# Kernel optimization log

Measured on AMD Instinct MI355X. Metric: run time of the kernel, lower is better.

## Reference

```python
import jax, jax.numpy as jnp
import numpy as np

FH, FW, CIN, COUT = 5, 5, 3, 16
PATCH = FH * FW * CIN  # 75
ALPHA = 1.0


def smooth_max(xk, axis):
    # alpha-softmax smooth maximum: sum(x * exp(alpha*x)) / sum(exp(alpha*x))
    w = jax.nn.softmax(ALPHA * xk, axis=axis)
    return jnp.sum(w * xk, axis=axis)


def setup_inputs() -> dict:
    key = jax.random.key(0)
    k_x, k_k1, k_k2 = jax.random.split(key, 3)
    B, Hout, Wout = 2, 220, 220
    x = jax.random.normal(k_x, (B, PATCH, Hout, Wout), dtype=jnp.float32)
    # xavier_uniform for kernel shape (fh, fw, cin, cout): fan_in=fh*fw*cin? torch treats
    # dims [..0]=fan stuff; a small uniform init is faithful enough for a numeric baseline.
    lim = float(np.sqrt(6.0 / (PATCH + COUT)))
    k1 = jax.random.uniform(k_k1, (FH, FW, CIN, COUT), jnp.float32, -lim, lim)
    k2 = jax.random.uniform(k_k2, (FH, FW, CIN, COUT), jnp.float32, -lim, lim)
    bias = jnp.zeros((COUT,), dtype=jnp.float32)
    return {"x": x, "k1": k1, "k2": k2, "bias": bias}


def reference(x, k1, k2, bias):
    # x: (B, patch_dim, Hout, Wout) unfolded patches
    k1f = k1.reshape(PATCH, COUT)  # (patch_dim, out_ch)
    k2f = k2.reshape(PATCH, COUT)
    # broadcast add: (B, patch_dim, out_ch, H, W)
    xk1 = x[:, :, None, :, :] + k1f[None, :, :, None, None]
    y11 = smooth_max(xk1, axis=1)  # (B, out_ch, H, W)
    xk2 = (-x)[:, :, None, :, :] + k2f[None, :, :, None, None]
    y22 = smooth_max(xk2, axis=1)
    return y11 + y22 + bias[None, :, None, None]
```

## Files before the change

### kernel.cpp

```cpp
#include <hip/hip_runtime.h>

#define HWD    48400
#define PATCHD 75
#define NPOS   96800

typedef __attribute__((ext_vector_type(8))) _Float16 f16x8;
typedef __attribute__((ext_vector_type(2))) __fp16   h16x2;
typedef __attribute__((ext_vector_type(4))) float    f32x4;

union U2 { h16x2 h; unsigned u; };
union UF { unsigned u[4]; f16x8 v; };

__global__ void smorph_build_tables(const float* __restrict__ k1,
                                    const float* __restrict__ k2,
                                    _Float16* __restrict__ tbl)
{
    int i = (int)blockIdx.x * 256 + (int)threadIdx.x;
    if (i >= 4 * 3 * 4 * 16 * 8) return;
    const int j = i & 7;
    const int c = (i >> 3) & 15;
    const int g = (i >> 7) & 3;
    const int t = i >> 9;
    const int s = t % 3;
    const int r = t / 3;
    const int k = 32 * s + 8 * g + j;
    float val = 0.f;
    if (k < PATCHD) {
        const float* kw = (r < 2) ? k1 : k2;
        const float w = kw[k * 16 + c];
        const float e = __expf(w);
        val = (r & 1) ? (w * e) : e;
    }
    tbl[i] = (_Float16)val;
}

__global__ __launch_bounds__(256, 4)
void smorph_mfma6(const float* __restrict__ x,
                  const _Float16* __restrict__ tbl,
                  const float* __restrict__ bias,
                  float* __restrict__ out)
{
    const int tid = (int)threadIdx.x;
    const int l   = tid & 63;
    const int w   = tid >> 6;
    const int g   = l >> 4;
    const int c   = l & 15;
    const int p0  = (int)blockIdx.x * 64 + w * 16;
    if (p0 >= NPOS) return;
    const int b   = (p0 >= HWD) ? 1 : 0;
    const int hw0 = p0 - b * HWD;

    const float* xb = x + (size_t)b * PATCHD * HWD + hw0 + c;
    const f16x8* tf = (const f16x8*)tbl;
    const int fbase = g * 16 + c;

    float xv[3][8];
    #pragma unroll
    for (int s = 0; s < 3; ++s)
        #pragma unroll
        for (int j = 0; j < 8; ++j) {
            int k = 32 * s + 8 * g + j;
            k = (k > PATCHD - 1) ? (PATCHD - 1) : k;
            xv[s][j] = xb[(size_t)k * HWD];
        }

    f32x4 aN1 = {0.f,0.f,0.f,0.f}, aD1 = {0.f,0.f,0.f,0.f};
    f32x4 aN2 = {0.f,0.f,0.f,0.f}, aD2 = {0.f,0.f,0.f,0.f};

    #pragma unroll
    for (int s = 0; s < 3; ++s) {
        const f16x8 a1f = tf[(0 * 3 + s) * 64 + fbase];
        const f16x8 b1f = tf[(1 * 3 + s) * 64 + fbase];
        const f16x8 a2f = tf[(2 * 3 + s) * 64 + fbase];
        const f16x8 b2f = tf[(3 * 3 + s) * 64 + fbase];

        float E[8], R[8];
        #pragma unroll
        for (int j = 0; j < 8; ++j) {
            E[j] = __expf(xv[s][j]);
            R[j] = __expf(-xv[s][j]);
        }

        UF fEx, fE, fRx, fR;
        #pragma unroll
        for (int jp = 0; jp < 4; ++jp) {
            const float x0 = xv[s][2*jp], x1 = xv[s][2*jp+1];
            U2 q;
            q.h = __builtin_amdgcn_cvt_pkrtz(E[2*jp] * x0,  E[2*jp+1] * x1);  fEx.u[jp] = q.u;
            q.h = __builtin_amdgcn_cvt_pkrtz(E[2*jp],       E[2*jp+1]);       fE.u[jp]  = q.u;
            q.h = __builtin_amdgcn_cvt_pkrtz(-R[2*jp] * x0, -R[2*jp+1] * x1); fRx.u[jp] = q.u;
            q.h = __builtin_amdgcn_cvt_pkrtz(R[2*jp],       R[2*jp+1]);       fR.u[jp]  = q.u;
        }

        aN1 = __builtin_amdgcn_mfma_f32_16x16x32_f16(a1f, fEx.v, aN1, 0, 0, 0);
        aN1 = __builtin_amdgcn_mfma_f32_16x16x32_f16(b1f, fE.v,  aN1, 0, 0, 0);
        aD1 = __builtin_amdgcn_mfma_f32_16x16x32_f16(a1f, fE.v,  aD1, 0, 0, 0);
        aN2 = __builtin_amdgcn_mfma_f32_16x16x32_f16(a2f, fRx.v, aN2, 0, 0, 0);
        aN2 = __builtin_amdgcn_mfma_f32_16x16x32_f16(b2f, fR.v,  aN2, 0, 0, 0);
        aD2 = __builtin_amdgcn_mfma_f32_16x16x32_f16(a2f, fR.v,  aD2, 0, 0, 0);
    }

    const float4 bsv = *(const float4*)(bias + 4 * g);
    float* ob = out + ((size_t)(b * 16 + 4 * g)) * HWD + hw0 + c;
    ob[0 * (size_t)HWD] = aN1[0] * __builtin_amdgcn_rcpf(aD1[0]) + aN2[0] * __builtin_amdgcn_rcpf(aD2[0]) + bsv.x;
    ob[1 * (size_t)HWD] = aN1[1] * __builtin_amdgcn_rcpf(aD1[1]) + aN2[1] * __builtin_amdgcn_rcpf(aD2[1]) + bsv.y;
    ob[2 * (size_t)HWD] = aN1[2] * __builtin_amdgcn_rcpf(aD1[2]) + aN2[2] * __builtin_amdgcn_rcpf(aD2[2]) + bsv.z;
    ob[3 * (size_t)HWD] = aN1[3] * __builtin_amdgcn_rcpf(aD1[3]) + aN2[3] * __builtin_amdgcn_rcpf(aD2[3]) + bsv.w;
}

extern "C" void kernel_launch(void* const* d_in, const int* in_sizes, int n_in,
                              void* d_out, int out_size, void* d_ws, size_t ws_size,
                              hipStream_t stream)
{
    const float* x    = (const float*)d_in[0];
    const float* k1   = (const float*)d_in[1];
    const float* k2   = (const float*)d_in[2];
    const float* bias = (const float*)d_in[3];
    float* out = (float*)d_out;
    _Float16* tbl = (_Float16*)d_ws;

    smorph_build_tables<<<(4 * 3 * 4 * 16 * 8 + 255) / 256, 256, 0, stream>>>(k1, k2, tbl);
    smorph_mfma6<<<(NPOS + 63) / 64, 256, 0, stream>>>(x, tbl, bias, out);
}
```

Measured before the change: 18.18 us.

## Convert to persistent grid-stride kernel with double-buffered x prefetch

Replaces the one-tile-per-block launch with a fixed grid of 512 persistent blocks that loop over tiles with a stride. Each block keeps the coefficient table fragments in registers and prefetches the next tile's x values into a second register buffer while it computes the current tile. The aim is to overlap global-load latency with exp and MFMA work and to stop reloading the table per tile. In exchange it uses more registers (occupancy hint lowered to 2) and gives load balancing over only about three tiles per block.

```diff
diff --git a/kernel.cpp b/kernel.cpp
--- a/kernel.cpp
+++ b/kernel.cpp
@@ -3,6 +3,8 @@
 #define HWD    48400
 #define PATCHD 75
 #define NPOS   96800
+#define NTILE  1513
+#define GRID   512
 
 typedef __attribute__((ext_vector_type(8))) _Float16 f16x8;
 typedef __attribute__((ext_vector_type(2))) __fp16   h16x2;
@@ -34,8 +36,8 @@
     tbl[i] = (_Float16)val;
 }
 
-__global__ __launch_bounds__(256, 4)
-void smorph_mfma6(const float* __restrict__ x,
+__global__ __launch_bounds__(256, 2)
+void smorph_mfma7(const float* __restrict__ x,
                   const _Float16* __restrict__ tbl,
                   const float* __restrict__ bias,
                   float* __restrict__ out)
@@ -45,67 +47,100 @@
     const int w   = tid >> 6;
     const int g   = l >> 4;
     const int c   = l & 15;
-    const int p0  = (int)blockIdx.x * 64 + w * 16;
-    if (p0 >= NPOS) return;
-    const int b   = (p0 >= HWD) ? 1 : 0;
-    const int hw0 = p0 - b * HWD;
 
-    const float* xb = x + (size_t)b * PATCHD * HWD + hw0 + c;
     const f16x8* tf = (const f16x8*)tbl;
     const int fbase = g * 16 + c;
+    f16x8 Tf[12];
+    #pragma unroll
+    for (int t = 0; t < 12; ++t) Tf[t] = tf[t * 64 + fbase];
 
-    float xv[3][8];
-    #pragma unroll
-    for (int s = 0; s < 3; ++s)
-        #pragma unroll
-        for (int j = 0; j < 8; ++j) {
-            int k = 32 * s + 8 * g + j;
-            k = (k > PATCHD - 1) ? (PATCHD - 1) : k;
-            xv[s][j] = xb[(size_t)k * HWD];
+    const float4 bsv = *(const float4*)(bias + 4 * g);
+
+    #define LOADX(dst, tt)                                                    \
+        {                                                                     \
+            int p0b_ = (tt) * 64;                                             \
+            if (p0b_ > NPOS - 64) p0b_ = NPOS - 64;                           \
+            const int p0_ = p0b_ + w * 16;                                    \
+            const int bb_ = (p0_ >= HWD) ? 1 : 0;                             \
+            const float* xb_ = x + (size_t)bb_ * PATCHD * HWD                 \
+                               + (p0_ - bb_ * HWD) + c;                       \
+            _Pragma("unroll")                                                 \
+            for (int s_ = 0; s_ < 3; ++s_)                                    \
+                _Pragma("unroll")                                             \
+                for (int j_ = 0; j_ < 8; ++j_) {                              \
+                    int k_ = 32 * s_ + 8 * g + j_;                            \
+                    k_ = (k_ > PATCHD - 1) ? (PATCHD - 1) : k_;               \
+                    (dst)[s_ * 8 + j_] = xb_[(size_t)k_ * HWD];               \
+                }                                                             \
         }
 
-    f32x4 aN1 = {0.f,0.f,0.f,0.f}, aD1 = {0.f,0.f,0.f,0.f};
-    f32x4 aN2 = {0.f,0.f,0.f,0.f}, aD2 = {0.f,0.f,0.f,0.f};
-
-    #pragma unroll
-    for (int s = 0; s < 3; ++s) {
-        const f16x8 a1f = tf[(0 * 3 + s) * 64 + fbase];
-        const f16x8 b1f = tf[(1 * 3 + s) * 64 + fbase];
-        const f16x8 a2f = tf[(2 * 3 + s) * 64 + fbase];
-        const f16x8 b2f = tf[(3 * 3 + s) * 64 + fbase];
-
-        float E[8], R[8];
-        #pragma unroll
-        for (int j = 0; j < 8; ++j) {
-            E[j] = __expf(xv[s][j]);
-            R[j] = __expf(-xv[s][j]);
+    #define COMPSTORE(src, tt)                                                \
+        {                                                                     \
+            f32x4 aN1 = {0.f,0.f,0.f,0.f}, aD1 = {0.f,0.f,0.f,0.f};          \
+            f32x4 aN2 = {0.f,0.f,0.f,0.f}, aD2 = {0.f,0.f,0.f,0.f};          \
+            _Pragma("unroll")                                                 \
+            for (int s_ = 0; s_ < 3; ++s_) {                                  \
+                float E[8], R[8];                                             \
+                _Pragma("unroll")                                             \
+                for (int j_ = 0; j_ < 8; ++j_) {                              \
+                    E[j_] = __expf((src)[s_ * 8 + j_]);                       \
+                    R[j_] = __expf(-(src)[s_ * 8 + j_]);                      \
+                }                                                             \
+                UF fEx, fE, fRx, fR;                                          \
+                _Pragma("unroll")                                             \
+                for (int jp = 0; jp < 4; ++jp) {                              \
+                    const float x0 = (src)[s_ * 8 + 2 * jp];                  \
+                    const float x1 = (src)[s_ * 8 + 2 * jp + 1];              \
+                    U2 q;                                                     \
+                    q.h = __builtin_amdgcn_cvt_pkrtz(E[2*jp] * x0,  E[2*jp+1] * x1);  fEx.u[jp] = q.u; \
+                    q.h = __builtin_amdgcn_cvt_pkrtz(E[2*jp],       E[2*jp+1]);       fE.u[jp]  = q.u; \
+                    q.h = __builtin_amdgcn_cvt_pkrtz(-R[2*jp] * x0, -R[2*jp+1] * x1); fRx.u[jp] = q.u; \
+                    q.h = __builtin_amdgcn_cvt_pkrtz(R[2*jp],       R[2*jp+1]);       fR.u[jp]  = q.u; \
+                }                                                             \
+                aN1 = __builtin_amdgcn_mfma_f32_16x16x32_f16(Tf[0 + s_], fEx.v, aN1, 0, 0, 0); \
+                aN1 = __builtin_amdgcn_mfma_f32_16x16x32_f16(Tf[3 + s_], fE.v,  aN1, 0, 0, 0); \
+                aD1 = __builtin_amdgcn_mfma_f32_16x16x32_f16(Tf[0 + s_], fE.v,  aD1, 0, 0, 0); \
+                aN2 = __builtin_amdgcn_mfma_f32_16x16x32_f16(Tf[6 + s_], fRx.v, aN2, 0, 0, 0); \
+                aN2 = __builtin_amdgcn_mfma_f32_16x16x32_f16(Tf[9 + s_], fR.v,  aN2, 0, 0, 0); \
+                aD2 = __builtin_amdgcn_mfma_f32_16x16x32_f16(Tf[6 + s_], fR.v,  aD2, 0, 0, 0); \
+            }                                                                 \
+            int p0b_ = (tt) * 64;                                             \
+            if (p0b_ > NPOS - 64) p0b_ = NPOS - 64;                           \
+            const int p0_ = p0b_ + w * 16;                                    \
+            const int bb_ = (p0_ >= HWD) ? 1 : 0;                             \
+            const int hw0_ = p0_ - bb_ * HWD;                                 \
+            float* ob_ = out + ((size_t)(bb_ * 16 + 4 * g)) * HWD + hw0_ + c; \
+            ob_[0 * (size_t)HWD] = aN1[0] * __builtin_amdgcn_rcpf(aD1[0]) + aN2[0] * __builtin_amdgcn_rcpf(aD2[0]) + bsv.x; \
+            ob_[1 * (size_t)HWD] = aN1[1] * __builtin_amdgcn_rcpf(aD1[1]) + aN2[1] * __builtin_amdgcn_rcpf(aD2[1]) + bsv.y; \
+            ob_[2 * (size_t)HWD] = aN1[2] * __builtin_amdgcn_rcpf(aD1[2]) + aN2[2] * __builtin_amdgcn_rcpf(aD2[2]) + bsv.z; \
+            ob_[3 * (size_t)HWD] = aN1[3] * __builtin_amdgcn_rcpf(aD1[3]) + aN2[3] * __builtin_amdgcn_rcpf(aD2[3]) + bsv.w; \
         }
 
-        UF fEx, fE, fRx, fR;
-        #pragma unroll
-        for (int jp = 0; jp < 4; ++jp) {
-            const float x0 = xv[s][2*jp], x1 = xv[s][2*jp+1];
-            U2 q;
-            q.h = __builtin_amdgcn_cvt_pkrtz(E[2*jp] * x0,  E[2*jp+1] * x1);  fEx.u[jp] = q.u;
-            q.h = __builtin_amdgcn_cvt_pkrtz(E[2*jp],       E[2*jp+1]);       fE.u[jp]  = q.u;
-            q.h = __builtin_amdgcn_cvt_pkrtz(-R[2*jp] * x0, -R[2*jp+1] * x1); fRx.u[jp] = q.u;
-            q.h = __builtin_amdgcn_cvt_pkrtz(R[2*jp],       R[2*jp+1]);       fR.u[jp]  = q.u;
+    float xva[24], xvb[24];
+    int t = (int)blockIdx.x;
+    LOADX(xva, t);
+    while (true) {
+        int tn = t + GRID;
+        if (tn < NTILE) {
+            LOADX(xvb, tn);
+            COMPSTORE(xva, t);
+            t = tn;
+        } else {
+            COMPSTORE(xva, t);
+            break;
         }
-
-        aN1 = __builtin_amdgcn_mfma_f32_16x16x32_f16(a1f, fEx.v, aN1, 0, 0, 0);
-        aN1 = __builtin_amdgcn_mfma_f32_16x16x32_f16(b1f, fE.v,  aN1, 0, 0, 0);
-        aD1 = __builtin_amdgcn_mfma_f32_16x16x32_f16(a1f, fE.v,  aD1, 0, 0, 0);
-        aN2 = __builtin_amdgcn_mfma_f32_16x16x32_f16(a2f, fRx.v, aN2, 0, 0, 0);
-        aN2 = __builtin_amdgcn_mfma_f32_16x16x32_f16(b2f, fR.v,  aN2, 0, 0, 0);
-        aD2 = __builtin_amdgcn_mfma_f32_16x16x32_f16(a2f, fR.v,  aD2, 0, 0, 0);
+        tn = t + GRID;
+        if (tn < NTILE) {
+            LOADX(xva, tn);
+            COMPSTORE(xvb, t);
+            t = tn;
+        } else {
+            COMPSTORE(xvb, t);
+            break;
+        }
     }
-
-    const float4 bsv = *(const float4*)(bias + 4 * g);
-    float* ob = out + ((size_t)(b * 16 + 4 * g)) * HWD + hw0 + c;
-    ob[0 * (size_t)HWD] = aN1[0] * __builtin_amdgcn_rcpf(aD1[0]) + aN2[0] * __builtin_amdgcn_rcpf(aD2[0]) + bsv.x;
-    ob[1 * (size_t)HWD] = aN1[1] * __builtin_amdgcn_rcpf(aD1[1]) + aN2[1] * __builtin_amdgcn_rcpf(aD2[1]) + bsv.y;
-    ob[2 * (size_t)HWD] = aN1[2] * __builtin_amdgcn_rcpf(aD1[2]) + aN2[2] * __builtin_amdgcn_rcpf(aD2[2]) + bsv.z;
-    ob[3 * (size_t)HWD] = aN1[3] * __builtin_amdgcn_rcpf(aD1[3]) + aN2[3] * __builtin_amdgcn_rcpf(aD2[3]) + bsv.w;
+    #undef LOADX
+    #undef COMPSTORE
 }
 
 extern "C" void kernel_launch(void* const* d_in, const int* in_sizes, int n_in,
@@ -120,5 +155,5 @@
     _Float16* tbl = (_Float16*)d_ws;
 
     smorph_build_tables<<<(4 * 3 * 4 * 16 * 8 + 255) / 256, 256, 0, stream>>>(k1, k2, tbl);
-    smorph_mfma6<<<(NPOS + 63) / 64, 256, 0, stream>>>(x, tbl, bias, out);
+    smorph_mfma7<<<GRID, 256, 0, stream>>>(x, tbl, bias, out);
 }
```

Measured after the change: 17.54 us. 1.04x faster.
